# Performance work log

Hardware: AMD Instinct MI355X
Metric: run time of the kernel (lower is better)

Reference implementation:

```python
import jax, jax.numpy as jnp
import numpy as np

HIDDEN = 128; HEADS = 8; HD = HIDDEN // HEADS; NRBF = 50; NLAYERS = 6
CUT = 5.0; MAXZ = 100
N = 5000; E = 100000


def cosine_cutoff(d):
    # cutoff_lower = 0: 0.5*(cos(pi*d/cut)+1) * (d < cut)
    return 0.5 * (jnp.cos(d * (jnp.pi / CUT)) + 1.0) * (d < CUT)


def expnorm_rbf(d, means, betas):
    # ExpNormalSmearing with cutoff_lower=0, alpha = 5/cutoff
    alpha = 5.0 / CUT
    return cosine_cutoff(d)[:, None] * jnp.exp(-betas * (jnp.exp(-alpha * d)[:, None] - means) ** 2)


def layernorm(x, w, b):
    m = x.mean(-1, keepdims=True)
    v = ((x - m) ** 2).mean(-1, keepdims=True)
    return (x - m) / jnp.sqrt(v + 1e-5) * w + b


def setup_inputs():
    key = jax.random.key(0)
    ks = jax.random.split(key, 16)
    start = float(np.exp(-CUT))

    def lin(k, fi, fo):
        return jax.random.normal(k, (fi, fo), jnp.float32) / np.sqrt(fi)

    def lin_l(k, fi, fo):
        return jax.random.normal(k, (NLAYERS, fi, fo), jnp.float32) / np.sqrt(fi)

    return {
        "z": jax.random.randint(ks[0], (N,), 0, MAXZ),
        "edge_index": jax.random.randint(ks[1], (2, E), 0, N),
        "edge_vec": jax.random.normal(ks[2], (E, 3), jnp.float32) * 1.7,
        "emb": jax.random.normal(ks[3], (MAXZ, HIDDEN), jnp.float32),
        "means": jnp.linspace(start, 1.0, NRBF, dtype=jnp.float32),
        "betas": jnp.full((NRBF,), (2.0 / NRBF * (1.0 - start)) ** -2, dtype=jnp.float32),
        "ne_emb": jax.random.normal(ks[4], (MAXZ, HIDDEN), jnp.float32),
        "dpW": lin(ks[5], NRBF, HIDDEN), "dpb": jnp.zeros((HIDDEN,), jnp.float32),
        "cbW": lin(ks[6], 2 * HIDDEN, HIDDEN), "cbb": jnp.zeros((HIDDEN,), jnp.float32),
        "lnw": jnp.ones((NLAYERS, HIDDEN), jnp.float32), "lnb": jnp.zeros((NLAYERS, HIDDEN), jnp.float32),
        "qW": lin_l(ks[7], HIDDEN, HIDDEN), "qb": jnp.zeros((NLAYERS, HIDDEN), jnp.float32),
        "kW": lin_l(ks[8], HIDDEN, HIDDEN), "kb": jnp.zeros((NLAYERS, HIDDEN), jnp.float32),
        "vW": lin_l(ks[9], HIDDEN, 3 * HIDDEN), "vb": jnp.zeros((NLAYERS, 3 * HIDDEN), jnp.float32),
        "oW": lin_l(ks[10], HIDDEN, 3 * HIDDEN), "ob": jnp.zeros((NLAYERS, 3 * HIDDEN), jnp.float32),
        "vecW": lin_l(ks[11], HIDDEN, 3 * HIDDEN),
        "dkW": lin_l(ks[12], NRBF, HIDDEN), "dkb": jnp.zeros((NLAYERS, HIDDEN), jnp.float32),
        "dvW": lin_l(ks[13], NRBF, 3 * HIDDEN), "dvb": jnp.zeros((NLAYERS, 3 * HIDDEN), jnp.float32),
        "onw": jnp.ones((HIDDEN,), jnp.float32), "onb": jnp.zeros((HIDDEN,), jnp.float32),
    }


def _forward(z, edge_index, edge_vec, emb, means, betas, ne_emb, dpW, dpb, cbW, cbb,
             lnw, lnb, qW, qb, kW, kb, vW, vb, oW, ob, vecW, dkW, dkb, dvW, dvb, onw, onb):
    src, dst = edge_index[0], edge_index[1]          # j (source), i (target)
    n = z.shape[0]
    x = emb[z]                                        # [N, H]
    ew = jnp.linalg.norm(edge_vec, axis=1)            # [E]
    ea = expnorm_rbf(ew, means, betas)                # [E, NRBF]
    nonself = src != dst
    # normalize edge vectors except self-loop edges (kept as-is, matching the torch clone/mask)
    evn = edge_vec / jnp.where(nonself, ew, 1.0)[:, None]
    cut_e = cosine_cutoff(ew)                         # [E]

    # --- NeighborEmbedding: self-loops removed from aggregation ---
    W = (ea @ dpW + dpb) * cut_e[:, None]
    W = jnp.where(nonself[:, None], W, 0.0)
    agg = jax.ops.segment_sum(ne_emb[z][src] * W, dst, num_segments=n)
    x = jnp.concatenate([x, agg], axis=1) @ cbW + cbb
    vec = jnp.zeros((n, 3, HIDDEN), x.dtype)

    def layer(carry, p):
        x, vec = carry
        h = layernorm(x, p["lnw"], p["lnb"])
        q = (h @ p["qW"] + p["qb"]).reshape(n, HEADS, HD)
        k = (h @ p["kW"] + p["kb"]).reshape(n, HEADS, HD)
        v = (h @ p["vW"] + p["vb"]).reshape(n, HEADS, 3 * HD)
        vec1, vec2, vec3 = jnp.split(jnp.einsum("nch,hk->nck", vec, p["vecW"]), 3, axis=-1)
        vec_dot = (vec1 * vec2).sum(axis=1)                    # [N, H]
        vec_h = vec.reshape(n, 3, HEADS, HD)
        dk = jax.nn.silu(ea @ p["dkW"] + p["dkb"]).reshape(-1, HEADS, HD)
        dv = jax.nn.silu(ea @ p["dvW"] + p["dvb"]).reshape(-1, HEADS, 3 * HD)
        # per-edge attention weight, silu activation, smoothly cut off
        attn = jax.nn.silu((q[dst] * k[src] * dk).sum(-1)) * cut_e[:, None]   # [E, heads]
        xm, w1, w2 = jnp.split(v[src] * dv, 3, axis=2)                        # each [E, heads, HD]
        xm = xm * attn[:, :, None]
        vecm = vec_h[src] * w1[:, None] + w2[:, None] * evn[:, :, None, None] # [E, 3, heads, HD]
        xa = jax.ops.segment_sum(xm, dst, num_segments=n).reshape(n, HIDDEN)
        va = jax.ops.segment_sum(vecm, dst, num_segments=n).reshape(n, 3, HIDDEN)
        o1, o2, o3 = jnp.split(xa @ p["oW"] + p["ob"], 3, axis=-1)
        dx = vec_dot * o2 + o3
        dvec = vec3 * o1[:, None, :] + va
        return (x + dx, vec + dvec), None

    stacked = {"lnw": lnw, "lnb": lnb, "qW": qW, "qb": qb, "kW": kW, "kb": kb,
               "vW": vW, "vb": vb, "oW": oW, "ob": ob, "vecW": vecW,
               "dkW": dkW, "dkb": dkb, "dvW": dvW, "dvb": dvb}
    (x, vec), _ = jax.lax.scan(layer, (x, vec), stacked)
    x = layernorm(x, onw, onb)
    return x, vec


def reference(z, edge_index, edge_vec, emb, means, betas, ne_emb, dpW, dpb, cbW, cbb,
              lnw, lnb, qW, qb, kW, kb, vW, vb, oW, ob, vecW, dkW, dkb, dvW, dvb, onw, onb):
    return _forward(z, edge_index, edge_vec, emb, means, betas, ne_emb, dpW, dpb, cbW, cbb,
                    lnw, lnb, qW, qb, kW, kb, vW, vb, oW, ob, vecW, dkW, dkb, dvW, dvb, onw, onb)
```

## Files before the change

### kernel.cpp

```cpp
#include <hip/hip_runtime.h>
#include <math.h>

#define HID 128
#define NRBF 50
#define NLAYERS 6
#define CUTV 5.0f
#define KNOTS 1024
#define TSCALE 204.8f
#define TINV   0.0048828125f
#define TROWS  (KNOTS + 1)
#define TSTRIDE ((size_t)TROWS * 512)
#define WCOLS 1408
#define KB 16

typedef unsigned int  uint32;
typedef unsigned short ushort16;
typedef __attribute__((ext_vector_type(8))) short short8;
typedef __attribute__((ext_vector_type(4))) float f32x4;

__device__ __forceinline__ float siluf(float x){ return x / (1.0f + __expf(-x)); }
__device__ __forceinline__ float lerpf(float a, float b, float f){ return fmaf(f, b - a, a); }
__device__ __forceinline__ ushort16 f2b(float x){
    uint32 u = __float_as_uint(x);
    u += 0x7fffu + ((u >> 16) & 1u);
    return (ushort16)(u >> 16);
}
__device__ __forceinline__ float b2f(ushort16 u){ return __uint_as_float(((uint32)u) << 16); }
__device__ __forceinline__ uint32 packp(float a, float b){
    return (uint32)f2b(a) | ((uint32)f2b(b) << 16);
}
__device__ __forceinline__ float plo(uint32 u){ return __uint_as_float(u << 16); }
__device__ __forceinline__ float phi(uint32 u){ return __uint_as_float(u & 0xffff0000u); }
__device__ __forceinline__ float plerp(uint32 u, float f){ float a = plo(u); return fmaf(f, phi(u) - a, a); }

__global__ void k_zero(int* p, int n){
    int i = blockIdx.x*blockDim.x + threadIdx.x;
    if (i < n) p[i] = 0;
}

__global__ void k_count(const int* ei, int E, int* counts){
    int e = blockIdx.x*blockDim.x + threadIdx.x;
    if (e < E) atomicAdd(&counts[ei[E + e]], 1);
}

__global__ void k_scan(const int* counts, int* offsets, int* cursor, int n){
    __shared__ int part[1024];
    int tid = threadIdx.x;
    int PER = (n + 1023) >> 10;
    int base = tid * PER;
    int loc[8]; int s = 0;
    #pragma unroll 8
    for (int ii = 0; ii < 8; ii++){
        if (ii < PER){
            int idx = base + ii;
            int c = (idx < n) ? counts[idx] : 0;
            loc[ii] = s; s += c;
        }
    }
    part[tid] = s;
    __syncthreads();
    for (int off = 1; off < 1024; off <<= 1){
        int v = (tid >= off) ? part[tid - off] : 0;
        __syncthreads();
        part[tid] += v;
        __syncthreads();
    }
    int excl = (tid == 0) ? 0 : part[tid - 1];
    #pragma unroll 8
    for (int ii = 0; ii < 8; ii++){
        if (ii < PER){
            int idx = base + ii;
            if (idx < n){ int o = excl + loc[ii]; offsets[idx] = o; cursor[idx] = o; }
        }
    }
    if (tid == 1023) offsets[n] = part[1023];
}

__global__ void k_scatter(const int* ei, int E, int* cursor, int* eperm){
    int e = blockIdx.x*blockDim.x + threadIdx.x;
    if (e < E){
        int d = ei[E + e];
        int pos = atomicAdd(&cursor[d], 1);
        eperm[pos] = e;
    }
}

__global__ void k_edge_vals(const int* ei, const float* edge_vec, const int* eperm, int E,
                            int4* edata, float4* evn4){
    int row = blockIdx.x*blockDim.x + threadIdx.x;
    if (row >= E) return;
    int e = eperm[row];
    int s = ei[e], d = ei[E + e];
    float vx = edge_vec[e*3+0], vy = edge_vec[e*3+1], vz = edge_vec[e*3+2];
    float ew = sqrtf(vx*vx + vy*vy + vz*vz);
    float cut = (ew < CUTV) ? 0.5f*(__cosf(ew * 0.62831853071795864f) + 1.0f) : 0.0f;
    int ns = (s != d) ? 1 : 0;
    float inv = ns ? (1.0f/ew) : 1.0f;
    float un = fminf(ew * TSCALE, (float)KNOTS);
    int j = (int)un;
    float f = un - (float)j;
    int4 ed; ed.x = s; ed.y = j; ed.z = __float_as_int(f); ed.w = __float_as_int(cut);
    edata[row] = ed;
    float4 ev; ev.x = vx*inv; ev.y = vy*inv; ev.z = vz*inv; ev.w = ns ? 1.0f : 0.0f;
    evn4[row] = ev;
}

__global__ void k_pad(ushort16* hb16, ushort16* vecm, ushort16* xab16, int N, int Nup, int N3up){
    int i = blockIdx.x*blockDim.x + threadIdx.x;
    int hpad = (Nup - N)*HID;
    int vpad = (N3up - 3*N)*HID;
    if (i < hpad){ hb16[(size_t)N*HID + i] = 0; xab16[(size_t)N*HID + i] = 0; }
    if (i < vpad) vecm[(size_t)3*N*HID + i] = 0;
}

__global__ __launch_bounds__(512) void k_build_tables(
    const float* means, const float* betas,
    const float* dkW, const float* dkb, const float* dvW, const float* dvb,
    uint32* Tp){
    int jb = blockIdx.x * KB;
    int l  = blockIdx.y;
    int c  = threadIdx.x;
    __shared__ float ea_s[KB+1][NRBF+2];
    for (int idx = c; idx < (KB+1)*NRBF; idx += 512){
        int kk = idx / NRBF, r = idx - kk*NRBF;
        float d = (jb + kk) * TINV;
        float cut = (d < CUTV) ? 0.5f*(__cosf(d * 0.62831853071795864f) + 1.0f) : 0.0f;
        float u = __expf(-d) - means[r];
        ea_s[kk][r] = cut * __expf(-betas[r]*u*u);
    }
    __syncthreads();
    const float* Wcol; int stride; float bias;
    if (c < HID){
        Wcol = dkW + (size_t)l*NRBF*HID + c; stride = HID;
        bias = dkb[(size_t)l*HID + c];
    } else {
        int cc = c - HID;
        int h = cc / 3, i = cc - h*3;
        int col = ((h >> 4)*48 + (h & 15)) + 16*i;
        Wcol = dvW + (size_t)l*NRBF*384 + col; stride = 384;
        bias = dvb[(size_t)l*384 + col];
    }
    float a[KB+1];
    #pragma unroll
    for (int k = 0; k <= KB; k++) a[k] = bias;
    for (int r = 0; r < NRBF; r++){
        float w = Wcol[(size_t)r*stride];
        #pragma unroll
        for (int k = 0; k <= KB; k++) a[k] += ea_s[k][r]*w;
    }
    uint32* dst = Tp + (size_t)l*TSTRIDE + (size_t)jb*512 + c;
    float sp = siluf(a[0]);
    #pragma unroll
    for (int k = 0; k < KB; k++){
        int j = jb + k;
        if (j >= TROWS) break;
        float sn = siluf(a[k+1]);
        dst[(size_t)k*512] = packp(sp, sn);
        sp = sn;
    }
}

__global__ __launch_bounds__(128) void k_build_ne(
    const float* means, const float* betas,
    const float* dpW, const float* dpb, float2* Tne){
    int j = blockIdx.x, c = threadIdx.x;
    __shared__ float ea0[NRBF], ea1[NRBF];
    float d0 = j * TINV, d1 = (j+1) * TINV;
    float c0 = (d0 < CUTV) ? 0.5f*(__cosf(d0 * 0.62831853071795864f) + 1.0f) : 0.0f;
    float c1 = (d1 < CUTV) ? 0.5f*(__cosf(d1 * 0.62831853071795864f) + 1.0f) : 0.0f;
    if (c < NRBF){
        float m = means[c], be = betas[c];
        float u0 = __expf(-d0) - m, u1 = __expf(-d1) - m;
        ea0[c] = c0 * __expf(-be*u0*u0);
        ea1[c] = c1 * __expf(-be*u1*u1);
    }
    __syncthreads();
    float a0 = dpb[c], a1 = a0;
    #pragma unroll
    for (int r = 0; r < NRBF; r++){ float w = dpW[r*HID + c]; a0 += ea0[r]*w; a1 += ea1[r]*w; }
    float2 o; o.x = a0*c0; o.y = a1*c1;
    Tne[(size_t)j*HID + c] = o;
}

__global__ __launch_bounds__(256) void k_build_wt(
    const float* qW, const float* kW, const float* vW, const float* vecW, const float* oW,
    ushort16* WT){
    int l = blockIdx.y; int c0 = blockIdx.x*32;
    const float* W; int C; int cs;
    if (c0 < 128)      { W = qW   + (size_t)l*HID*128; C = 128; cs = c0; }
    else if (c0 < 256) { W = kW   + (size_t)l*HID*128; C = 128; cs = c0-128; }
    else if (c0 < 640) { W = vW   + (size_t)l*HID*384; C = 384; cs = c0-256; }
    else if (c0 < 1024){ W = vecW + (size_t)l*HID*384; C = 384; cs = c0-640; }
    else               { W = oW   + (size_t)l*HID*384; C = 384; cs = c0-1024; }
    __shared__ ushort16 t[128][33];
    for (int i = threadIdx.x; i < 128*32; i += 256){
        int k = i >> 5, c = i & 31;
        t[k][c] = f2b(W[(size_t)k*C + cs + c]);
    }
    __syncthreads();
    ushort16* dst = WT + (size_t)l*WCOLS*HID + (size_t)c0*HID;
    for (int i = threadIdx.x; i < 128*32; i += 256){
        int c = i >> 7, k = i & 127;
        dst[(size_t)c*HID + k] = t[k][c];
    }
}

__global__ __launch_bounds__(256) void k_mfma01(
    const ushort16* __restrict__ hb16, const ushort16* __restrict__ vecm,
    const ushort16* __restrict__ WT,
    const float* __restrict__ qbias, const float* __restrict__ kbias, const float* __restrict__ vbias,
    float* __restrict__ qo, ushort16* __restrict__ ko, ushort16* __restrict__ vo,
    ushort16* __restrict__ vecout, int N){
    int cg = blockIdx.x;
    int rblk = blockIdx.y*64;
    const ushort16* A; int R; int cblk; const ushort16* wt;
    if (cg < 10){ A = hb16; R = N;   cblk = cg*64;      wt = WT; }
    else        { A = vecm; R = 3*N; cblk = (cg-10)*64; wt = WT + (size_t)640*HID; }
    if (rblk >= R) return;
    int wave = threadIdx.x >> 6, lane = threadIdx.x & 63;
    int r0 = rblk + wave*16;
    int l16 = lane & 15, lg = lane >> 4;
    short8 a[4];
    const ushort16* ar = A + (size_t)(r0 + l16)*HID + lg*8;
    #pragma unroll
    for (int ks = 0; ks < 4; ks++) a[ks] = *(const short8*)(ar + ks*32);
    f32x4 acc[4];
    #pragma unroll
    for (int ct = 0; ct < 4; ct++){ acc[ct][0]=0.f; acc[ct][1]=0.f; acc[ct][2]=0.f; acc[ct][3]=0.f; }
    #pragma unroll
    for (int ct = 0; ct < 4; ct++){
        const ushort16* br = wt + (size_t)(cblk + ct*16 + l16)*HID + lg*8;
        #pragma unroll
        for (int ks = 0; ks < 4; ks++){
            short8 b = *(const short8*)(br + ks*32);
            acc[ct] = __builtin_amdgcn_mfma_f32_16x16x32_bf16(a[ks], b, acc[ct], 0, 0, 0);
        }
    }
    #pragma unroll
    for (int ct = 0; ct < 4; ct++){
        int gc = cblk + ct*16 + l16;
        #pragma unroll
        for (int rg = 0; rg < 4; rg++){
            int row = r0 + lg*4 + rg;
            if (row >= R) continue;
            float v = acc[ct][rg];
            if (cg < 10){
                if (gc < 128)      qo[(size_t)row*HID + gc]       = v + qbias[gc];
                else if (gc < 256) ko[(size_t)row*HID + (gc-128)] = f2b(v + kbias[gc-128]);
                else               vo[(size_t)row*384 + (gc-256)] = f2b(v + vbias[gc-256]);
            } else {
                vecout[(size_t)row*384 + gc] = f2b(v);
            }
        }
    }
}

__global__ __launch_bounds__(256) void k_mfma_o(
    const ushort16* __restrict__ A, const ushort16* __restrict__ WT,
    const float* __restrict__ bias, float* __restrict__ out, int N){
    int cblk = blockIdx.x*64;
    int rblk = blockIdx.y*64;
    if (rblk >= N) return;
    int wave = threadIdx.x >> 6, lane = threadIdx.x & 63;
    int r0 = rblk + wave*16;
    int l16 = lane & 15, lg = lane >> 4;
    short8 a[4];
    const ushort16* ar = A + (size_t)(r0 + l16)*HID + lg*8;
    #pragma unroll
    for (int ks = 0; ks < 4; ks++) a[ks] = *(const short8*)(ar + ks*32);
    f32x4 acc[4];
    #pragma unroll
    for (int ct = 0; ct < 4; ct++){ acc[ct][0]=0.f; acc[ct][1]=0.f; acc[ct][2]=0.f; acc[ct][3]=0.f; }
    const ushort16* wt = WT + (size_t)1024*HID;
    #pragma unroll
    for (int ct = 0; ct < 4; ct++){
        const ushort16* br = wt + (size_t)(cblk + ct*16 + l16)*HID + lg*8;
        #pragma unroll
        for (int ks = 0; ks < 4; ks++){
            short8 b = *(const short8*)(br + ks*32);
            acc[ct] = __builtin_amdgcn_mfma_f32_16x16x32_bf16(a[ks], b, acc[ct], 0, 0, 0);
        }
    }
    #pragma unroll
    for (int ct = 0; ct < 4; ct++){
        int gc = cblk + ct*16 + l16;
        float bb = bias[gc];
        #pragma unroll
        for (int rg = 0; rg < 4; rg++){
            int row = r0 + lg*4 + rg;
            if (row >= N) continue;
            out[(size_t)row*384 + gc] = acc[ct][rg] + bb;
        }
    }
}

__global__ __launch_bounds__(128) void k_ne_agg(
    const int* offsets, const int4* edata, const float4* evn4, const float2* Tne,
    const int* z, const float* ne_emb, float* agg){
    int i = blockIdx.x, h = threadIdx.x;
    float acc = 0.f;
    int r0 = offsets[i], r1 = offsets[i+1];
    #pragma unroll 4
    for (int row = r0; row < r1; row++){
        int4 ed = edata[row];
        int s = ed.x, j = ed.y;
        float f = __int_as_float(ed.z);
        float mask = evn4[row].w;
        float2 tv = Tne[(size_t)j*HID + h];
        float w = lerpf(tv.x, tv.y, f) * mask;
        acc += w * ne_emb[(size_t)z[s]*HID + h];
    }
    agg[(size_t)i*HID + h] = acc;
}

__global__ __launch_bounds__(128) void k_combine_ln(
    const int* z, const float* emb, const float* agg, const float* cbW, const float* cbb,
    const float* lnw0, const float* lnb0,
    float* x, ushort16* hb16, float* vec, ushort16* vecm, int N){
    int n0 = blockIdx.x*8, h = threadIdx.x;
    __shared__ float in_s[8][2*HID];
    int nr = min(8, N - n0);
    for (int m = 0; m < nr; m++){
        in_s[m][h]       = emb[(size_t)z[n0+m]*HID + h];
        in_s[m][HID + h] = agg[(size_t)(n0+m)*HID + h];
    }
    __syncthreads();
    float acc[8];
    #pragma unroll
    for (int m = 0; m < 8; m++) acc[m] = 0.f;
    for (int kk = 0; kk < 2*HID; kk += 4){
        float w0 = cbW[(kk+0)*HID + h], w1 = cbW[(kk+1)*HID + h];
        float w2 = cbW[(kk+2)*HID + h], w3 = cbW[(kk+3)*HID + h];
        #pragma unroll
        for (int m = 0; m < 8; m++){
            const float* a = &in_s[m][kk];
            acc[m] += a[0]*w0 + a[1]*w1 + a[2]*w2 + a[3]*w3;
        }
    }
    float bias = cbb[h], w = lnw0[h], bb = lnb0[h];
    __shared__ float r1_[2], r2_[2];
    int wid = h >> 6;
    for (int m = 0; m < nr; m++){
        int n = n0 + m;
        float v = acc[m] + bias;
        x[(size_t)n*HID + h] = v;
        float s1 = v, s2 = v*v;
        #pragma unroll
        for (int o = 32; o; o >>= 1){ s1 += __shfl_xor(s1, o, 64); s2 += __shfl_xor(s2, o, 64); }
        if ((h & 63) == 0){ r1_[wid] = s1; r2_[wid] = s2; }
        __syncthreads();
        float sum = r1_[0] + r1_[1], sumsq = r2_[0] + r2_[1];
        float mean = sum * (1.f/HID);
        float var = sumsq * (1.f/HID) - mean*mean;
        float inv = rsqrtf(var + 1e-5f);
        hb16[(size_t)n*HID + h] = f2b((v - mean)*inv*w + bb);
        __syncthreads();
        vec [(size_t)n*384 + h]       = 0.f;
        vec [(size_t)n*384 + 128 + h] = 0.f;
        vec [(size_t)n*384 + 256 + h] = 0.f;
        vecm[(size_t)n*384 + h]       = 0;
        vecm[(size_t)n*384 + 128 + h] = 0;
        vecm[(size_t)n*384 + 256 + h] = 0;
    }
}

__global__ __launch_bounds__(128) void k_edge_agg(
    const int* __restrict__ offsets, const int4* __restrict__ edata,
    const float4* __restrict__ evn4, const uint32* __restrict__ Tp,
    const float* __restrict__ q, const ushort16* __restrict__ kb16,
    const ushort16* __restrict__ vb16, const ushort16* __restrict__ vecm,
    ushort16* __restrict__ xa16, float* __restrict__ va){
    int i = blockIdx.x, h = threadIdx.x;
    int head = h >> 4;
    int c0 = head*48 + (h & 15);
    float qv = q[(size_t)i*HID + h];
    float axa = 0.f, av0 = 0.f, av1 = 0.f, av2 = 0.f;
    int r0 = offsets[i], r1 = offsets[i+1];
    for (int t0 = r0; t0 < r1; t0 += 4){
        float f_[4], cut_[4], ex_[4], ey_[4], ez_[4];
        uint32 tdk_[4], tdv0_[4], tdv1_[4], tdv2_[4];
        ushort16 kv_[4], v0_[4], v1_[4], v2_[4], vc0_[4], vc1_[4], vc2_[4];
        #pragma unroll
        for (int u = 0; u < 4; u++){
            int row = min(t0 + u, r1 - 1);
            int4 ed = edata[row];
            int s = ed.x, j = ed.y;
            f_[u]   = __int_as_float(ed.z);
            cut_[u] = __int_as_float(ed.w);
            const uint32* tp = Tp + (size_t)j*512;
            tdk_[u]  = tp[h];
            const uint32* q3 = tp + 128 + 3*h;
            tdv0_[u] = q3[0];
            tdv1_[u] = q3[1];
            tdv2_[u] = q3[2];
            kv_[u] = kb16[(size_t)s*HID + h];
            const ushort16* vr = vb16 + (size_t)s*384;
            v0_[u] = vr[c0]; v1_[u] = vr[c0+16]; v2_[u] = vr[c0+32];
            const ushort16* vc = vecm + (size_t)s*384;
            vc0_[u] = vc[h]; vc1_[u] = vc[128+h]; vc2_[u] = vc[256+h];
            float4 ev = evn4[row];
            ex_[u] = ev.x; ey_[u] = ev.y; ez_[u] = ev.z;
        }
        #pragma unroll
        for (int u = 0; u < 4; u++){
            if (t0 + u >= r1) break;
            float f = f_[u];
            float dk = plerp(tdk_[u], f);
            float p = qv * b2f(kv_[u]) * dk;
            p += __shfl_xor(p, 1, 64);
            p += __shfl_xor(p, 2, 64);
            p += __shfl_xor(p, 4, 64);
            p += __shfl_xor(p, 8, 64);
            float attn = siluf(p) * cut_[u];
            float dv0 = plerp(tdv0_[u], f);
            float dv1 = plerp(tdv1_[u], f);
            float dv2 = plerp(tdv2_[u], f);
            axa += b2f(v0_[u]) * dv0 * attn;
            float w1v = b2f(v1_[u]) * dv1;
            float w2v = b2f(v2_[u]) * dv2;
            av0 += b2f(vc0_[u])*w1v + w2v*ex_[u];
            av1 += b2f(vc1_[u])*w1v + w2v*ey_[u];
            av2 += b2f(vc2_[u])*w1v + w2v*ez_[u];
        }
    }
    xa16[(size_t)i*HID + h] = f2b(axa);
    va[(size_t)i*384 + h]       = av0;
    va[(size_t)i*384 + 128 + h] = av1;
    va[(size_t)i*384 + 256 + h] = av2;
}

__global__ __launch_bounds__(128) void k_update_ln(
    float* __restrict__ x, float* __restrict__ vec, ushort16* __restrict__ vecm,
    const float* __restrict__ o, const ushort16* __restrict__ vecout, const float* __restrict__ va,
    const float* __restrict__ lnw_n, const float* __restrict__ lnb_n,
    ushort16* __restrict__ hb16, float* __restrict__ outx, float* __restrict__ outv, int fin){
    int n = blockIdx.x, h = threadIdx.x;
    const ushort16* vo = vecout + (size_t)n*1152;
    float vdot = b2f(vo[h])*b2f(vo[128+h]) + b2f(vo[384+h])*b2f(vo[512+h])
               + b2f(vo[768+h])*b2f(vo[896+h]);
    const float* on = o + (size_t)n*384;
    float xv = x[(size_t)n*HID + h] + vdot*on[128 + h] + on[256 + h];
    float o1 = on[h];
    size_t vb = (size_t)n*384;
    float v0 = vec[vb + h]       + b2f(vo[256  + h])*o1 + va[vb + h];
    float v1 = vec[vb + 128 + h] + b2f(vo[640  + h])*o1 + va[vb + 128 + h];
    float v2 = vec[vb + 256 + h] + b2f(vo[1024 + h])*o1 + va[vb + 256 + h];
    float s1 = xv, s2 = xv*xv;
    #pragma unroll
    for (int oo = 32; oo; oo >>= 1){ s1 += __shfl_xor(s1, oo, 64); s2 += __shfl_xor(s2, oo, 64); }
    __shared__ float r1_[2], r2_[2];
    int wid = h >> 6;
    if ((h & 63) == 0){ r1_[wid] = s1; r2_[wid] = s2; }
    __syncthreads();
    float sum = r1_[0] + r1_[1], sumsq = r2_[0] + r2_[1];
    float mean = sum * (1.f/HID);
    float var = sumsq * (1.f/HID) - mean*mean;
    float inv = rsqrtf(var + 1e-5f);
    float lnv = (xv - mean)*inv*lnw_n[h] + lnb_n[h];
    if (!fin){
        x[(size_t)n*HID + h] = xv;
        vec[vb + h] = v0; vec[vb + 128 + h] = v1; vec[vb + 256 + h] = v2;
        vecm[vb + h] = f2b(v0); vecm[vb + 128 + h] = f2b(v1); vecm[vb + 256 + h] = f2b(v2);
        hb16[(size_t)n*HID + h] = f2b(lnv);
    } else {
        outx[(size_t)n*HID + h] = lnv;
        outv[vb + h] = v0; outv[vb + 128 + h] = v1; outv[vb + 256 + h] = v2;
    }
}

extern "C" void kernel_launch(void* const* d_in, const int* in_sizes, int n_in,
                              void* d_out, int out_size, void* d_ws, size_t ws_size,
                              hipStream_t stream){
    const int*   z        = (const int*)  d_in[0];
    const int*   ei       = (const int*)  d_in[1];
    const float* edge_vec = (const float*)d_in[2];
    const float* emb      = (const float*)d_in[3];
    const float* means    = (const float*)d_in[4];
    const float* betas    = (const float*)d_in[5];
    const float* ne_emb   = (const float*)d_in[6];
    const float* dpW      = (const float*)d_in[7];
    const float* dpb      = (const float*)d_in[8];
    const float* cbW      = (const float*)d_in[9];
    const float* cbb      = (const float*)d_in[10];
    const float* lnw      = (const float*)d_in[11];
    const float* lnb      = (const float*)d_in[12];
    const float* qW       = (const float*)d_in[13];
    const float* qb       = (const float*)d_in[14];
    const float* kW       = (const float*)d_in[15];
    const float* kb       = (const float*)d_in[16];
    const float* vW       = (const float*)d_in[17];
    const float* vb       = (const float*)d_in[18];
    const float* oW       = (const float*)d_in[19];
    const float* obias    = (const float*)d_in[20];
    const float* vecW     = (const float*)d_in[21];
    const float* dkW      = (const float*)d_in[22];
    const float* dkb      = (const float*)d_in[23];
    const float* dvW      = (const float*)d_in[24];
    const float* dvb      = (const float*)d_in[25];
    const float* onw      = (const float*)d_in[26];
    const float* onb      = (const float*)d_in[27];

    int N = in_sizes[0];
    int E = in_sizes[1] / 2;
    int Nup  = ((N + 63) >> 6) << 6;
    int N3up = ((3*N + 63) >> 6) << 6;

    char* p = (char*)d_ws;
    auto alloc = [&](size_t bytes){ void* r = (void*)p; p += (bytes + 255) & ~(size_t)255; return r; };
    int*      counts  = (int*)     alloc((size_t)N*4);
    int*      offsets = (int*)     alloc((size_t)(N+1)*4);
    int*      cursor  = (int*)     alloc((size_t)N*4);
    int*      eperm   = (int*)     alloc((size_t)E*4);
    int4*     edata   = (int4*)    alloc((size_t)E*16);
    float4*   evn4    = (float4*)  alloc((size_t)E*16);
    uint32*   Tp      = (uint32*)  alloc((size_t)NLAYERS*TSTRIDE*4);
    float2*   Tne     = (float2*)  alloc((size_t)TROWS*HID*8);
    ushort16* WT      = (ushort16*)alloc((size_t)NLAYERS*WCOLS*HID*2);
    float*    agg     = (float*)   alloc((size_t)N*HID*4);
    float*    xb      = (float*)   alloc((size_t)N*HID*4);
    ushort16* hb16    = (ushort16*)alloc((size_t)Nup*HID*2);
    float*    qb_     = (float*)   alloc((size_t)N*HID*4);
    ushort16* kb16    = (ushort16*)alloc((size_t)N*HID*2);
    ushort16* vb16    = (ushort16*)alloc((size_t)N*384*2);
    ushort16* vecm    = (ushort16*)alloc((size_t)N3up*HID*2);
    float*    vecb    = (float*)   alloc((size_t)N*384*4);
    ushort16* vecout  = (ushort16*)alloc((size_t)N*1152*2);
    ushort16* xab16   = (ushort16*)alloc((size_t)Nup*HID*2);
    float*    vab     = (float*)   alloc((size_t)N*384*4);
    float*    ob_     = (float*)   alloc((size_t)N*384*4);

    k_zero<<<(N+255)/256, 256, 0, stream>>>(counts, N);
    k_count<<<(E+255)/256, 256, 0, stream>>>(ei, E, counts);
    k_scan<<<1, 1024, 0, stream>>>(counts, offsets, cursor, N);
    k_scatter<<<(E+255)/256, 256, 0, stream>>>(ei, E, cursor, eperm);
    k_edge_vals<<<(E+255)/256, 256, 0, stream>>>(ei, edge_vec, eperm, E, edata, evn4);
    k_pad<<<((Nup-N)*HID + (N3up-3*N)*HID + 255)/256 + 1, 256, 0, stream>>>(hb16, vecm, xab16, N, Nup, N3up);

    k_build_tables<<<dim3((TROWS + KB - 1)/KB, NLAYERS), 512, 0, stream>>>(means, betas, dkW, dkb, dvW, dvb, Tp);
    k_build_ne<<<TROWS, 128, 0, stream>>>(means, betas, dpW, dpb, Tne);
    k_build_wt<<<dim3(WCOLS/32, NLAYERS), 256, 0, stream>>>(qW, kW, vW, vecW, oW, WT);
    k_ne_agg<<<N, 128, 0, stream>>>(offsets, edata, evn4, Tne, z, ne_emb, agg);
    k_combine_ln<<<(N+7)/8, 128, 0, stream>>>(z, emb, agg, cbW, cbb, lnw, lnb,
                                              xb, hb16, vecb, vecm, N);

    float* outx = (float*)d_out;
    float* outv = (float*)d_out + (size_t)N*HID;

    for (int l = 0; l < NLAYERS; l++){
        const ushort16* WTl = WT + (size_t)l*WCOLS*HID;
        k_mfma01<<<dim3(16, (3*N+63)/64), 256, 0, stream>>>(hb16, vecm, WTl,
            qb + (size_t)l*HID, kb + (size_t)l*HID, vb + (size_t)l*384,
            qb_, kb16, vb16, vecout, N);
        k_edge_agg<<<N, 128, 0, stream>>>(offsets, edata, evn4, Tp + (size_t)l*TSTRIDE,
                                          qb_, kb16, vb16, vecm, xab16, vab);
        k_mfma_o<<<dim3(6, (N+63)/64), 256, 0, stream>>>(xab16, WTl, obias + (size_t)l*384, ob_, N);
        int fin = (l == NLAYERS-1);
        k_update_ln<<<N, 128, 0, stream>>>(xb, vecb, vecm, ob_, vecout, vab,
            fin ? onw : lnw + (size_t)(l+1)*HID,
            fin ? onb : lnb + (size_t)(l+1)*HID,
            hb16, outx, outv, fin);
    }
}
```

Baseline: 682.6 us.

## Fuse output projection into LN update, pad table rows, double-buffer edge loads

Merges the output-projection MFMA with the residual/layernorm update kernel, so the per-layer o buffer stays in shared memory instead of being written to and reread from global memory. Pads each table row to four words per head channel so the value-table entries can be fetched with one 16-byte load. Restructures the edge aggregation loop into a two-stage software pipeline (A/B register sets) so loads for the next four edges are in flight while the current four are computed. This costs more registers and a large shared buffer in the fused kernel, and that kernel has far fewer blocks than before.

```diff
diff --git a/kernel.cpp b/kernel.cpp
--- a/kernel.cpp
+++ b/kernel.cpp
@@ -9,7 +9,8 @@
 #define TSCALE 204.8f
 #define TINV   0.0048828125f
 #define TROWS  (KNOTS + 1)
-#define TSTRIDE ((size_t)TROWS * 512)
+#define TRWORDS 640
+#define TSTRIDE ((size_t)TROWS * TRWORDS)
 #define WCOLS 1408
 #define KB 16
 
@@ -129,16 +130,19 @@
         ea_s[kk][r] = cut * __expf(-betas[r]*u*u);
     }
     __syncthreads();
-    const float* Wcol; int stride; float bias;
+    const float* Wcol; int stride; float bias; int slot; int pad3 = 0;
     if (c < HID){
         Wcol = dkW + (size_t)l*NRBF*HID + c; stride = HID;
         bias = dkb[(size_t)l*HID + c];
+        slot = c;
     } else {
         int cc = c - HID;
         int h = cc / 3, i = cc - h*3;
         int col = ((h >> 4)*48 + (h & 15)) + 16*i;
         Wcol = dvW + (size_t)l*NRBF*384 + col; stride = 384;
         bias = dvb[(size_t)l*384 + col];
+        slot = 128 + 4*h + i;
+        pad3 = (i == 2) ? 1 : 0;
     }
     float a[KB+1];
     #pragma unroll
@@ -148,14 +152,15 @@
         #pragma unroll
         for (int k = 0; k <= KB; k++) a[k] += ea_s[k][r]*w;
     }
-    uint32* dst = Tp + (size_t)l*TSTRIDE + (size_t)jb*512 + c;
+    uint32* dst = Tp + (size_t)l*TSTRIDE + (size_t)jb*TRWORDS + slot;
     float sp = siluf(a[0]);
     #pragma unroll
     for (int k = 0; k < KB; k++){
         int j = jb + k;
         if (j >= TROWS) break;
         float sn = siluf(a[k+1]);
-        dst[(size_t)k*512] = packp(sp, sn);
+        dst[(size_t)k*TRWORDS] = packp(sp, sn);
+        if (pad3) dst[(size_t)k*TRWORDS + 1] = 0;
         sp = sn;
     }
 }
@@ -255,45 +260,6 @@
     }
 }
 
-__global__ __launch_bounds__(256) void k_mfma_o(
-    const ushort16* __restrict__ A, const ushort16* __restrict__ WT,
-    const float* __restrict__ bias, float* __restrict__ out, int N){
-    int cblk = blockIdx.x*64;
-    int rblk = blockIdx.y*64;
-    if (rblk >= N) return;
-    int wave = threadIdx.x >> 6, lane = threadIdx.x & 63;
-    int r0 = rblk + wave*16;
-    int l16 = lane & 15, lg = lane >> 4;
-    short8 a[4];
-    const ushort16* ar = A + (size_t)(r0 + l16)*HID + lg*8;
-    #pragma unroll
-    for (int ks = 0; ks < 4; ks++) a[ks] = *(const short8*)(ar + ks*32);
-    f32x4 acc[4];
-    #pragma unroll
-    for (int ct = 0; ct < 4; ct++){ acc[ct][0]=0.f; acc[ct][1]=0.f; acc[ct][2]=0.f; acc[ct][3]=0.f; }
-    const ushort16* wt = WT + (size_t)1024*HID;
-    #pragma unroll
-    for (int ct = 0; ct < 4; ct++){
-        const ushort16* br = wt + (size_t)(cblk + ct*16 + l16)*HID + lg*8;
-        #pragma unroll
-        for (int ks = 0; ks < 4; ks++){
-            short8 b = *(const short8*)(br + ks*32);
-            acc[ct] = __builtin_amdgcn_mfma_f32_16x16x32_bf16(a[ks], b, acc[ct], 0, 0, 0);
-        }
-    }
-    #pragma unroll
-    for (int ct = 0; ct < 4; ct++){
-        int gc = cblk + ct*16 + l16;
-        float bb = bias[gc];
-        #pragma unroll
-        for (int rg = 0; rg < 4; rg++){
-            int row = r0 + lg*4 + rg;
-            if (row >= N) continue;
-            out[(size_t)row*384 + gc] = acc[ct][rg] + bb;
-        }
-    }
-}
-
 __global__ __launch_bounds__(128) void k_ne_agg(
     const int* offsets, const int4* edata, const float4* evn4, const float2* Tne,
     const int* z, const float* ne_emb, float* agg){
@@ -364,6 +330,49 @@
     }
 }
 
+struct EB {
+    float f, cut, ex, ey, ez;
+    uint32 tdk, td0, td1, td2;
+    ushort16 kv, v0, v1, v2, vc0, vc1, vc2;
+};
+
+__device__ __forceinline__ void eb_load(EB& b, int row, int h, int c0,
+    const int4* edata, const float4* evn4, const uint32* Tp,
+    const ushort16* kb16, const ushort16* vb16, const ushort16* vecm){
+    int4 ed = edata[row];
+    int s = ed.x, j = ed.y;
+    b.f = __int_as_float(ed.z); b.cut = __int_as_float(ed.w);
+    float4 ev = evn4[row];
+    b.ex = ev.x; b.ey = ev.y; b.ez = ev.z;
+    const uint32* tp = Tp + (size_t)j*TRWORDS;
+    b.tdk = tp[h];
+    uint4 q4 = *(const uint4*)(tp + 128 + 4*h);
+    b.td0 = q4.x; b.td1 = q4.y; b.td2 = q4.z;
+    b.kv = kb16[(size_t)s*HID + h];
+    const ushort16* vr = vb16 + (size_t)s*384;
+    b.v0 = vr[c0]; b.v1 = vr[c0+16]; b.v2 = vr[c0+32];
+    const ushort16* vc = vecm + (size_t)s*384;
+    b.vc0 = vc[h]; b.vc1 = vc[128+h]; b.vc2 = vc[256+h];
+}
+
+__device__ __forceinline__ void eb_comp(const EB& b, float qv,
+    float& axa, float& av0, float& av1, float& av2){
+    float f = b.f;
+    float dk = plerp(b.tdk, f);
+    float p = qv * b2f(b.kv) * dk;
+    p += __shfl_xor(p, 1, 64);
+    p += __shfl_xor(p, 2, 64);
+    p += __shfl_xor(p, 4, 64);
+    p += __shfl_xor(p, 8, 64);
+    float attn = siluf(p) * b.cut;
+    axa += b2f(b.v0) * plerp(b.td0, f) * attn;
+    float w1v = b2f(b.v1) * plerp(b.td1, f);
+    float w2v = b2f(b.v2) * plerp(b.td2, f);
+    av0 += b2f(b.vc0)*w1v + w2v*b.ex;
+    av1 += b2f(b.vc1)*w1v + w2v*b.ey;
+    av2 += b2f(b.vc2)*w1v + w2v*b.ez;
+}
+
 __global__ __launch_bounds__(128) void k_edge_agg(
     const int* __restrict__ offsets, const int4* __restrict__ edata,
     const float4* __restrict__ evn4, const uint32* __restrict__ Tp,
@@ -373,54 +382,33 @@
     int i = blockIdx.x, h = threadIdx.x;
     int head = h >> 4;
     int c0 = head*48 + (h & 15);
-    float qv = q[(size_t)i*HID + h];
+    int r0 = offsets[i], r1 = offsets[i+1];
     float axa = 0.f, av0 = 0.f, av1 = 0.f, av2 = 0.f;
-    int r0 = offsets[i], r1 = offsets[i+1];
-    for (int t0 = r0; t0 < r1; t0 += 4){
-        float f_[4], cut_[4], ex_[4], ey_[4], ez_[4];
-        uint32 tdk_[4], tdv0_[4], tdv1_[4], tdv2_[4];
-        ushort16 kv_[4], v0_[4], v1_[4], v2_[4], vc0_[4], vc1_[4], vc2_[4];
-        #pragma unroll
-        for (int u = 0; u < 4; u++){
-            int row = min(t0 + u, r1 - 1);
-            int4 ed = edata[row];
-            int s = ed.x, j = ed.y;
-            f_[u]   = __int_as_float(ed.z);
-            cut_[u] = __int_as_float(ed.w);
-            const uint32* tp = Tp + (size_t)j*512;
-            tdk_[u]  = tp[h];
-            const uint32* q3 = tp + 128 + 3*h;
-            tdv0_[u] = q3[0];
-            tdv1_[u] = q3[1];
-            tdv2_[u] = q3[2];
-            kv_[u] = kb16[(size_t)s*HID + h];
-            const ushort16* vr = vb16 + (size_t)s*384;
-            v0_[u] = vr[c0]; v1_[u] = vr[c0+16]; v2_[u] = vr[c0+32];
-            const ushort16* vc = vecm + (size_t)s*384;
-            vc0_[u] = vc[h]; vc1_[u] = vc[128+h]; vc2_[u] = vc[256+h];
-            float4 ev = evn4[row];
-            ex_[u] = ev.x; ey_[u] = ev.y; ez_[u] = ev.z;
-        }
-        #pragma unroll
-        for (int u = 0; u < 4; u++){
-            if (t0 + u >= r1) break;
-            float f = f_[u];
-            float dk = plerp(tdk_[u], f);
-            float p = qv * b2f(kv_[u]) * dk;
-            p += __shfl_xor(p, 1, 64);
-            p += __shfl_xor(p, 2, 64);
-            p += __shfl_xor(p, 4, 64);
-            p += __shfl_xor(p, 8, 64);
-            float attn = siluf(p) * cut_[u];
-            float dv0 = plerp(tdv0_[u], f);
-            float dv1 = plerp(tdv1_[u], f);
-            float dv2 = plerp(tdv2_[u], f);
-            axa += b2f(v0_[u]) * dv0 * attn;
-            float w1v = b2f(v1_[u]) * dv1;
-            float w2v = b2f(v2_[u]) * dv2;
-            av0 += b2f(vc0_[u])*w1v + w2v*ex_[u];
-            av1 += b2f(vc1_[u])*w1v + w2v*ey_[u];
-            av2 += b2f(vc2_[u])*w1v + w2v*ez_[u];
+    if (r0 < r1){
+        float qv = q[(size_t)i*HID + h];
+        int last = r1 - 1;
+        EB A0, A1, A2, A3, B0, B1, B2, B3;
+        eb_load(A0, min(r0+0, last), h, c0, edata, evn4, Tp, kb16, vb16, vecm);
+        eb_load(A1, min(r0+1, last), h, c0, edata, evn4, Tp, kb16, vb16, vecm);
+        eb_load(A2, min(r0+2, last), h, c0, edata, evn4, Tp, kb16, vb16, vecm);
+        eb_load(A3, min(r0+3, last), h, c0, edata, evn4, Tp, kb16, vb16, vecm);
+        for (int t0 = r0; t0 < r1; t0 += 8){
+            eb_load(B0, min(t0+4, last), h, c0, edata, evn4, Tp, kb16, vb16, vecm);
+            eb_load(B1, min(t0+5, last), h, c0, edata, evn4, Tp, kb16, vb16, vecm);
+            eb_load(B2, min(t0+6, last), h, c0, edata, evn4, Tp, kb16, vb16, vecm);
+            eb_load(B3, min(t0+7, last), h, c0, edata, evn4, Tp, kb16, vb16, vecm);
+            eb_comp(A0, qv, axa, av0, av1, av2);
+            if (t0+1 < r1) eb_comp(A1, qv, axa, av0, av1, av2);
+            if (t0+2 < r1) eb_comp(A2, qv, axa, av0, av1, av2);
+            if (t0+3 < r1) eb_comp(A3, qv, axa, av0, av1, av2);
+            eb_load(A0, min(t0+8,  last), h, c0, edata, evn4, Tp, kb16, vb16, vecm);
+            eb_load(A1, min(t0+9,  last), h, c0, edata, evn4, Tp, kb16, vb16, vecm);
+            eb_load(A2, min(t0+10, last), h, c0, edata, evn4, Tp, kb16, vb16, vecm);
+            eb_load(A3, min(t0+11, last), h, c0, edata, evn4, Tp, kb16, vb16, vecm);
+            if (t0+4 < r1) eb_comp(B0, qv, axa, av0, av1, av2);
+            if (t0+5 < r1) eb_comp(B1, qv, axa, av0, av1, av2);
+            if (t0+6 < r1) eb_comp(B2, qv, axa, av0, av1, av2);
+            if (t0+7 < r1) eb_comp(B3, qv, axa, av0, av1, av2);
         }
     }
     xa16[(size_t)i*HID + h] = f2b(axa);
@@ -429,42 +417,89 @@
     va[(size_t)i*384 + 256 + h] = av2;
 }
 
-__global__ __launch_bounds__(128) void k_update_ln(
+#define OROWS 32
+__global__ __launch_bounds__(256) void k_oupd(
+    const ushort16* __restrict__ xab16, const ushort16* __restrict__ WT,
+    const float* __restrict__ obias,
     float* __restrict__ x, float* __restrict__ vec, ushort16* __restrict__ vecm,
-    const float* __restrict__ o, const ushort16* __restrict__ vecout, const float* __restrict__ va,
+    const ushort16* __restrict__ vecout, const float* __restrict__ va,
     const float* __restrict__ lnw_n, const float* __restrict__ lnb_n,
-    ushort16* __restrict__ hb16, float* __restrict__ outx, float* __restrict__ outv, int fin){
-    int n = blockIdx.x, h = threadIdx.x;
-    const ushort16* vo = vecout + (size_t)n*1152;
-    float vdot = b2f(vo[h])*b2f(vo[128+h]) + b2f(vo[384+h])*b2f(vo[512+h])
-               + b2f(vo[768+h])*b2f(vo[896+h]);
-    const float* on = o + (size_t)n*384;
-    float xv = x[(size_t)n*HID + h] + vdot*on[128 + h] + on[256 + h];
-    float o1 = on[h];
-    size_t vb = (size_t)n*384;
-    float v0 = vec[vb + h]       + b2f(vo[256  + h])*o1 + va[vb + h];
-    float v1 = vec[vb + 128 + h] + b2f(vo[640  + h])*o1 + va[vb + 128 + h];
-    float v2 = vec[vb + 256 + h] + b2f(vo[1024 + h])*o1 + va[vb + 256 + h];
-    float s1 = xv, s2 = xv*xv;
-    #pragma unroll
-    for (int oo = 32; oo; oo >>= 1){ s1 += __shfl_xor(s1, oo, 64); s2 += __shfl_xor(s2, oo, 64); }
-    __shared__ float r1_[2], r2_[2];
-    int wid = h >> 6;
-    if ((h & 63) == 0){ r1_[wid] = s1; r2_[wid] = s2; }
+    ushort16* __restrict__ hb16, float* __restrict__ outx, float* __restrict__ outv,
+    int N, int fin){
+    __shared__ float o_s[OROWS][385];
+    int tile = blockIdx.x; int r0 = tile*OROWS;
+    int wid = threadIdx.x >> 6, lane = threadIdx.x & 63;
+    int l16 = lane & 15, lg = lane >> 4;
+    {
+        int rr = r0 + (wid & 1)*16;
+        const ushort16* ar = xab16 + (size_t)(rr + l16)*HID + lg*8;
+        short8 a[4];
+        #pragma unroll
+        for (int ks = 0; ks < 4; ks++) a[ks] = *(const short8*)(ar + ks*32);
+        int cbase = (wid >> 1)*192;
+        const ushort16* wt = WT + (size_t)1024*HID;
+        #pragma unroll
+        for (int ct = 0; ct < 12; ct++){
+            f32x4 acc; acc[0]=0.f; acc[1]=0.f; acc[2]=0.f; acc[3]=0.f;
+            const ushort16* br = wt + (size_t)(cbase + ct*16 + l16)*HID + lg*8;
+            #pragma unroll
+            for (int ks = 0; ks < 4; ks++){
+                short8 b = *(const short8*)(br + ks*32);
+                acc = __builtin_amdgcn_mfma_f32_16x16x32_bf16(a[ks], b, acc, 0, 0, 0);
+            }
+            int gc = cbase + ct*16 + l16;
+            float bb = obias[gc];
+            #pragma unroll
+            for (int rg = 0; rg < 4; rg++)
+                o_s[(wid & 1)*16 + lg*4 + rg][gc] = acc[rg] + bb;
+        }
+    }
     __syncthreads();
-    float sum = r1_[0] + r1_[1], sumsq = r2_[0] + r2_[1];
-    float mean = sum * (1.f/HID);
-    float var = sumsq * (1.f/HID) - mean*mean;
-    float inv = rsqrtf(var + 1e-5f);
-    float lnv = (xv - mean)*inv*lnw_n[h] + lnb_n[h];
-    if (!fin){
-        x[(size_t)n*HID + h] = xv;
-        vec[vb + h] = v0; vec[vb + 128 + h] = v1; vec[vb + 256 + h] = v2;
-        vecm[vb + h] = f2b(v0); vecm[vb + 128 + h] = f2b(v1); vecm[vb + 256 + h] = f2b(v2);
-        hb16[(size_t)n*HID + h] = f2b(lnv);
-    } else {
-        outx[(size_t)n*HID + h] = lnv;
-        outv[vb + h] = v0; outv[vb + 128 + h] = v1; outv[vb + 256 + h] = v2;
+    for (int pass = 0; pass < 8; pass++){
+        int nrow = pass*4 + wid;
+        int n = r0 + nrow;
+        if (n >= N) break;
+        const ushort16* vo = vecout + (size_t)n*1152;
+        const float* o_r = o_s[nrow];
+        size_t vb = (size_t)n*384;
+        float xva, xvb, v0a, v0b, v1a, v1b, v2a, v2b;
+        #pragma unroll
+        for (int half = 0; half < 2; half++){
+            int hh = lane + half*64;
+            float vdot = b2f(vo[hh])*b2f(vo[128+hh]) + b2f(vo[384+hh])*b2f(vo[512+hh])
+                       + b2f(vo[768+hh])*b2f(vo[896+hh]);
+            float o1 = o_r[hh], o2 = o_r[128+hh], o3 = o_r[256+hh];
+            float xv = x[(size_t)n*HID + hh] + vdot*o2 + o3;
+            float v0 = vec[vb + hh]       + b2f(vo[256  + hh])*o1 + va[vb + hh];
+            float v1 = vec[vb + 128 + hh] + b2f(vo[640  + hh])*o1 + va[vb + 128 + hh];
+            float v2 = vec[vb + 256 + hh] + b2f(vo[1024 + hh])*o1 + va[vb + 256 + hh];
+            if (half == 0){ xva = xv; v0a = v0; v1a = v1; v2a = v2; }
+            else          { xvb = xv; v0b = v0; v1b = v1; v2b = v2; }
+        }
+        float s1 = xva + xvb, s2 = xva*xva + xvb*xvb;
+        #pragma unroll
+        for (int o = 32; o; o >>= 1){ s1 += __shfl_xor(s1, o, 64); s2 += __shfl_xor(s2, o, 64); }
+        float mean = s1 * (1.f/HID);
+        float var = s2 * (1.f/HID) - mean*mean;
+        float inv = rsqrtf(var + 1e-5f);
+        #pragma unroll
+        for (int half = 0; half < 2; half++){
+            int hh = lane + half*64;
+            float xv = half ? xvb : xva;
+            float v0 = half ? v0b : v0a;
+            float v1 = half ? v1b : v1a;
+            float v2 = half ? v2b : v2a;
+            float lnv = (xv - mean)*inv*lnw_n[hh] + lnb_n[hh];
+            if (!fin){
+                x[(size_t)n*HID + hh] = xv;
+                vec[vb + hh] = v0; vec[vb + 128 + hh] = v1; vec[vb + 256 + hh] = v2;
+                vecm[vb + hh] = f2b(v0); vecm[vb + 128 + hh] = f2b(v1); vecm[vb + 256 + hh] = f2b(v2);
+                hb16[(size_t)n*HID + hh] = f2b(lnv);
+            } else {
+                outx[(size_t)n*HID + hh] = lnv;
+                outv[vb + hh] = v0; outv[vb + 128 + hh] = v1; outv[vb + 256 + hh] = v2;
+            }
+        }
     }
 }
 
@@ -527,7 +562,6 @@
     ushort16* vecout  = (ushort16*)alloc((size_t)N*1152*2);
     ushort16* xab16   = (ushort16*)alloc((size_t)Nup*HID*2);
     float*    vab     = (float*)   alloc((size_t)N*384*4);
-    float*    ob_     = (float*)   alloc((size_t)N*384*4);
 
     k_zero<<<(N+255)/256, 256, 0, stream>>>(counts, N);
     k_count<<<(E+255)/256, 256, 0, stream>>>(ei, E, counts);
@@ -553,11 +587,11 @@
             qb_, kb16, vb16, vecout, N);
         k_edge_agg<<<N, 128, 0, stream>>>(offsets, edata, evn4, Tp + (size_t)l*TSTRIDE,
                                           qb_, kb16, vb16, vecm, xab16, vab);
-        k_mfma_o<<<dim3(6, (N+63)/64), 256, 0, stream>>>(xab16, WTl, obias + (size_t)l*384, ob_, N);
         int fin = (l == NLAYERS-1);
-        k_update_ln<<<N, 128, 0, stream>>>(xb, vecb, vecm, ob_, vecout, vab,
+        k_oupd<<<(N + OROWS - 1)/OROWS, 256, 0, stream>>>(xab16, WTl, obias + (size_t)l*384,
+            xb, vecb, vecm, vecout, vab,
             fin ? onw : lnw + (size_t)(l+1)*HID,
             fin ? onb : lnb + (size_t)(l+1)*HID,
-            hb16, outx, outv, fin);
-    }
-}
+            hb16, outx, outv, N, fin);
+    }
+}
```

After: 692.6 us. Within noise of the previous version (+1.5%).
